# Kernel tuning notes

Hardware: AMD Instinct MI355X
Metric: run time of the kernel (lower is better)

Reference implementation:

```python
import jax, jax.numpy as jnp
import numpy as np

WS = 7
HEADS = 8
DIM = 96
MLP_HIDDEN = 384


def _rel_pos_index(ws):
    coords = np.stack(np.meshgrid(np.arange(ws), np.arange(ws), indexing='ij'))  # (2,ws,ws)
    cf = coords.reshape(2, -1)
    rel = (cf[:, :, None] - cf[:, None, :]).transpose(1, 2, 0).copy()  # (N,N,2)
    rel[..., 0] += ws - 1
    rel[..., 1] += ws - 1
    rel[..., 0] *= 2 * ws - 1
    return rel.sum(-1)  # (N,N)

RPI = jnp.asarray(_rel_pos_index(WS).reshape(-1))


def _window_partition(x, ws):
    B, H, W, C = x.shape
    x = x.reshape(B, H // ws, ws, W // ws, ws, C)
    return x.transpose(0, 1, 3, 2, 4, 5).reshape(-1, ws, ws, C)


def _window_reverse(w, ws, H, W):
    B = w.shape[0] // ((H // ws) * (W // ws))
    x = w.reshape(B, H // ws, W // ws, ws, ws, -1)
    return x.transpose(0, 1, 3, 2, 4, 5).reshape(B, H, W, -1)


def _ln(x, g, b, eps=1e-5):
    m = jnp.mean(x, -1, keepdims=True)
    v = jnp.mean(jnp.square(x - m), -1, keepdims=True)
    return (x - m) * jax.lax.rsqrt(v + eps) * g + b


def _bn(x, g, b, m, v, eps=1e-5):
    # inference-mode BatchNorm2d over NCHW
    s = (g * jax.lax.rsqrt(v + eps))[None, :, None, None]
    return (x - m[None, :, None, None]) * s + b[None, :, None, None]


def _conv(x, w, pad, dil):
    return jax.lax.conv_general_dilated(
        x, w, (1, 1), [(pad, pad), (pad, pad)], rhs_dilation=(dil, dil),
        dimension_numbers=('NCHW', 'OIHW', 'NCHW'))


def forward_impl(x, ndwi_mask, norm1_g, norm1_b, qkv_w, qkv_b, proj_w, proj_b, rpb_table,
                 norm2_g, norm2_b, mlp_w1, mlp_b1, mlp_w2, mlp_b2, norm3_g, norm3_b,
                 conv1_w, conv1_b, bn1_g, bn1_b, bn1_m, bn1_v,
                 conv2_w, conv2_b, bn2_g, bn2_b, bn2_m, bn2_v, H, W):
    B, L, C = x.shape
    ws, heads = WS, HEADS
    shift = ws // 2  # +3 forward shift ('se' direction)
    shortcut = x
    xn = _ln(x, norm1_g, norm1_b).reshape(B, H, W, C)
    sx = jnp.roll(xn, (shift, shift), axis=(1, 2))
    # NDWI-derived additive attention mask (same-region pairs -> 0, else -100)
    nm = jnp.roll(ndwi_mask[:, 0], (shift, shift), axis=(1, 2))  # (B,H,W)
    mw = _window_partition(nm[..., None], ws).reshape(-1, ws * ws)  # (B*nW, N)
    diff = mw[:, None, :] - mw[:, :, None]  # (B*nW, N, N) = mw[:,j]-mw[:,i]
    attn_mask = jnp.where(diff != 0, jnp.float32(-100.0), jnp.float32(0.0)).astype(x.dtype)
    # windowed attention
    xw = _window_partition(sx, ws).reshape(-1, ws * ws, C)
    B_, N, _ = xw.shape
    hd = C // heads
    qkv = (xw @ qkv_w.T + qkv_b).reshape(B_, N, 3, heads, hd).transpose(2, 0, 3, 1, 4)
    q, k, v = qkv[0] * (hd ** -0.5), qkv[1], qkv[2]  # (B_,h,N,hd)
    attn = jnp.einsum('bhnd,bhmd->bhnm', q, k)
    bias = rpb_table[RPI].reshape(N, N, heads).transpose(2, 0, 1)  # (h,N,N)
    attn = attn + bias[None] + attn_mask[:, None]
    attn = jax.nn.softmax(attn, axis=-1)
    out = jnp.einsum('bhnm,bhmd->bhnd', attn, v).transpose(0, 2, 1, 3).reshape(B_, N, C)
    out = out @ proj_w.T + proj_b
    sx = _window_reverse(out.reshape(-1, ws, ws, C), ws, H, W)
    rshift = -ws // 2  # == -4 for ws=7, matches torch's asymmetric reverse shift
    x = jnp.roll(sx, (rshift, rshift), axis=(1, 2)).reshape(B, H * W, C)
    x = shortcut + x
    # MLP
    h = _ln(x, norm2_g, norm2_b)
    h = jax.nn.gelu(h @ mlp_w1.T + mlp_b1, approximate=False) @ mlp_w2.T + mlp_b2
    x = x + h
    # multi-scale CNN branch
    shortcut2 = x
    img = _ln(x, norm3_g, norm3_b).transpose(0, 2, 1).reshape(B, C, H, W)
    h = _conv(img, conv1_w, 1, 1) + conv1_b[None, :, None, None]
    h = jax.nn.gelu(_bn(h, bn1_g, bn1_b, bn1_m, bn1_v), approximate=False)
    h = _conv(h, conv2_w, 2, 2) + conv2_b[None, :, None, None]
    h = jax.nn.gelu(_bn(h, bn2_g, bn2_b, bn2_m, bn2_v), approximate=False)
    h = h.reshape(B, C, H * W).transpose(0, 2, 1)
    return shortcut2 + h


def setup_inputs() -> dict:
    key = jax.random.key(0)
    k = jax.random.split(key, 10)
    B, H, W, C, hid = 4, 224, 224, DIM, MLP_HIDDEN
    std = 0.02
    f32 = jnp.float32
    return {
        'x': jax.random.normal(k[0], (B, H * W, C), f32),
        'ndwi_mask': jax.random.randint(k[1], (B, 1, H, W), 0, 2).astype(f32),
        'norm1_g': jnp.ones((C,), f32), 'norm1_b': jnp.zeros((C,), f32),
        'qkv_w': jax.random.normal(k[2], (3 * C, C), f32) * std, 'qkv_b': jnp.zeros((3 * C,), f32),
        'proj_w': jax.random.normal(k[3], (C, C), f32) * std, 'proj_b': jnp.zeros((C,), f32),
        'rpb_table': jax.random.normal(k[4], ((2 * WS - 1) ** 2, HEADS), f32) * std,
        'norm2_g': jnp.ones((C,), f32), 'norm2_b': jnp.zeros((C,), f32),
        'mlp_w1': jax.random.normal(k[5], (hid, C), f32) * std, 'mlp_b1': jnp.zeros((hid,), f32),
        'mlp_w2': jax.random.normal(k[6], (C, hid), f32) * std, 'mlp_b2': jnp.zeros((C,), f32),
        'norm3_g': jnp.ones((C,), f32), 'norm3_b': jnp.zeros((C,), f32),
        'conv1_w': jax.random.normal(k[7], (C, C, 3, 3), f32) * std, 'conv1_b': jnp.zeros((C,), f32),
        'bn1_g': jnp.ones((C,), f32), 'bn1_b': jnp.zeros((C,), f32),
        'bn1_m': jnp.zeros((C,), f32), 'bn1_v': jnp.ones((C,), f32),
        'conv2_w': jax.random.normal(k[8], (C, C, 3, 3), f32) * std, 'conv2_b': jnp.zeros((C,), f32),
        'bn2_g': jnp.ones((C,), f32), 'bn2_b': jnp.zeros((C,), f32),
        'bn2_m': jnp.zeros((C,), f32), 'bn2_v': jnp.ones((C,), f32),
        'H': H, 'W': W,
    }


def reference(x, ndwi_mask, norm1_g, norm1_b, qkv_w, qkv_b, proj_w, proj_b, rpb_table,
              norm2_g, norm2_b, mlp_w1, mlp_b1, mlp_w2, mlp_b2, norm3_g, norm3_b,
              conv1_w, conv1_b, bn1_g, bn1_b, bn1_m, bn1_v,
              conv2_w, conv2_b, bn2_g, bn2_b, bn2_m, bn2_v, H, W):
    return forward_impl(x, ndwi_mask, norm1_g, norm1_b, qkv_w, qkv_b, proj_w, proj_b, rpb_table,
                        norm2_g, norm2_b, mlp_w1, mlp_b1, mlp_w2, mlp_b2, norm3_g, norm3_b,
                        conv1_w, conv1_b, bn1_g, bn1_b, bn1_m, bn1_v,
                        conv2_w, conv2_b, bn2_g, bn2_b, bn2_m, bn2_v, H, W)
```

## Files before the change

kernel.cpp:

```cpp
#include <hip/hip_runtime.h>
#include <hip/hip_bf16.h>

typedef unsigned int u32;
typedef unsigned short u16;

#define DF __device__ __forceinline__

DF float bf2f(u16 v){ u32 t = ((u32)v)<<16; return __builtin_bit_cast(float, t); }
DF u16 f2bf(float f){
  u32 t = __builtin_bit_cast(u32, f);
  t += 0x7fffu + ((t>>16)&1u);
  return (u16)(t>>16);
}
DF float lo16(u32 p){ return __builtin_bit_cast(float, p<<16); }
DF float hi16(u32 p){ return __builtin_bit_cast(float, p & 0xffff0000u); }
DF u32 pack2(float a, float b){ return (u32)f2bf(a) | (((u32)f2bf(b))<<16); }
DF float gelu(float x){ return 0.5f*x*(1.0f+erff(x*0.70710678118654752f)); }

#if defined(__has_builtin)
#if __has_builtin(__builtin_amdgcn_fdot2_f32_bf16)
#define HAVE_DOT2 1
#endif
#endif
#ifdef HAVE_DOT2
DF float dot2bf(u32 a, u32 b, float c){
  typedef __bf16 b2 __attribute__((ext_vector_type(2)));
  return __builtin_amdgcn_fdot2_f32_bf16(__builtin_bit_cast(b2,a), __builtin_bit_cast(b2,b), c, false);
}
#else
DF float dot2bf(u32 a, u32 b, float c){
  float d;
  asm("v_dot2_f32_bf16 %0, %1, %2, %3" : "=v"(d) : "v"(a), "v"(b), "v"(c));
  return d;
}
#endif

typedef __attribute__((ext_vector_type(8))) __bf16 bf16x8;
typedef __attribute__((ext_vector_type(4))) float f32x4;

__global__ void wprep_k(const float* __restrict__ qkvw, const float* __restrict__ projw,
                        u32* __restrict__ w8q, u32* __restrict__ w8p)
{
  int e = blockIdx.x*256 + threadIdx.x;
  if (e < 13824){
    int jk = e >> 8, lane = (e >> 2) & 63, q = e & 3;
    int jt = jk/3, ks = jk - jt*3;
    int n = jt*16 + (lane & 15);
    int k = ks*32 + (lane >> 4)*8 + 2*q;
    w8q[e] = pack2(qkvw[n*96 + k], qkvw[n*96 + k + 1]);
  } else if (e < 18432){
    int r2 = e - 13824;
    int jk = r2 >> 8, lane = (r2 >> 2) & 63, q = r2 & 3;
    int jt = jk/3, ks = jk - jt*3;
    int n = jt*16 + (lane & 15);
    int k = ks*32 + (lane >> 4)*8 + 2*q;
    w8p[r2] = pack2(projw[n*96 + k], projw[n*96 + k + 1]);
  }
}

__global__ void wprep_cv(const float* __restrict__ c1w, const float* __restrict__ c2w,
                         u32* __restrict__ wcv)
{
  int e = blockIdx.x*256 + threadIdx.x;
  if (e >= 82944) return;
  int conv = e / 41472, r = e - conv*41472;
  int tap = r / 4608, r2 = r - tap*4608;
  int jk = r2 >> 8;
  int lane = (r2 >> 2) & 63;
  int q = r2 & 3;
  int j = jk/3, ks = jk - j*3;
  int n = j*16 + (lane & 15);
  int k = ks*32 + (lane >> 4)*8 + 2*q;
  const float* s = conv ? c2w : c1w;
  wcv[e] = pack2(s[(n*96 + k)*9 + tap], s[(n*96 + k + 1)*9 + tap]);
}

__global__ void wprep_m(const float* __restrict__ w1, const float* __restrict__ w2,
                        u32* __restrict__ wm)
{
  int e = blockIdx.x*256 + threadIdx.x;
  if (e >= 36864) return;
  int which = e / 18432, r = e - which*18432;
  int q = r / 4608, r2 = r - q*4608;
  int jk = r2 >> 8, lane = (r2 >> 2) & 63, qq = r2 & 3;
  int jt = jk/3, ks = jk - jt*3;
  int n = jt*16 + (lane & 15);
  int k = ks*32 + (lane >> 4)*8 + 2*qq;
  if (which == 0){
    const float* s = w1 + (size_t)(q*96 + n)*96 + k;
    wm[e] = pack2(s[0], s[1]);
  } else {
    const float* s = w2 + (size_t)n*384 + q*96 + k;
    wm[e] = pack2(s[0], s[1]);
  }
}

__global__ __launch_bounds__(256,3) void attn_k(
    const float* __restrict__ x, const float* __restrict__ ndwi,
    const float* __restrict__ n1g, const float* __restrict__ n1b,
    const u32* __restrict__ w8q, const float* __restrict__ qb,
    const u32* __restrict__ w8p, const float* __restrict__ pb,
    const float* __restrict__ rpbt, u16* __restrict__ x1o)
{
  __shared__ __align__(16) u16 xA[4*3*64*8];
  __shared__ u32 qp[49*49];
  __shared__ u32 kp[49*49];
  __shared__ u16 vpT[96*50];
  __shared__ float rpb[8*169];
  __shared__ float mw[49];
  const int tid = threadIdx.x;
  const int blk = blockIdx.x;
  const int b = blk >> 10, wy = (blk>>5)&31, wx = blk&31;
  const int wv_ = __builtin_amdgcn_readfirstlane(tid >> 6);
  const int ln  = tid & 63;
  const int colv = ln & 15, rgrp = ln >> 4;

  for (int i = tid; i < 1352; i += 256){
    int h = i/169, idx = i - h*169;
    rpb[i] = rpbt[idx*8 + h];
  }
  for (int i = tid; i < 96; i += 256) vpT[i*50 + 49] = 0;

  if (tid < 196){
    const int t = tid >> 2, p = tid & 3;
    const int ty = t/7, tx = t - (t/7)*7;
    int sy = wy*7 + ty - 3; if (sy < 0) sy += 224;
    int sx = wx*7 + tx - 3; if (sx < 0) sx += 224;
    const size_t rowb = ((size_t)((b*224 + sy)*224 + sx))*96;
    const float* xr = x + rowb + p*24;
    float c[24];
    #pragma unroll
    for (int q = 0; q < 6; q++){
      float4 v = ((const float4*)xr)[q];
      c[q*4+0]=v.x; c[q*4+1]=v.y; c[q*4+2]=v.z; c[q*4+3]=v.w;
    }
    if (p == 0) mw[t] = ndwi[(size_t)b*50176 + sy*224 + sx];
    float s = 0.f, s2 = 0.f;
    #pragma unroll
    for (int j = 0; j < 24; j++){ s += c[j]; s2 += c[j]*c[j]; }
    s  += __shfl_xor(s, 1);  s  += __shfl_xor(s, 2);
    s2 += __shfl_xor(s2, 1); s2 += __shfl_xor(s2, 2);
    float m = s*(1.f/96.f);
    float rs = rsqrtf(s2*(1.f/96.f) - m*m + 1e-5f);
    const int mt = t >> 4, row = t & 15;
    #pragma unroll
    for (int jj = 0; jj < 12; jj++){
      int k = p*24 + 2*jj;
      float a = (c[2*jj]  -m)*rs*n1g[k]   + n1b[k];
      float d = (c[2*jj+1]-m)*rs*n1g[k+1] + n1b[k+1];
      int ks = k >> 5, g = (k & 31) >> 3, i = k & 7;
      *(u32*)&xA[(((mt*3 + ks)*64 + g*16 + row)<<3) + i] = pack2(a, d);
    }
  }
  __syncthreads();

  {
    bf16x8 af[3];
    #pragma unroll
    for (int ks = 0; ks < 3; ks++)
      af[ks] = *(const bf16x8*)&xA[((wv_*3 + ks)*64 + ln)*8];
    u16* qpu = (u16*)qp;
    u16* kpu = (u16*)kp;
    const float S = 0.28867513459481287f;
    for (int jt = 0; jt < 18; jt++){
      f32x4 c = (f32x4){0.f,0.f,0.f,0.f};
      #pragma unroll
      for (int ks = 0; ks < 3; ks++){
        bf16x8 bw = *(const bf16x8*)(w8q + ((jt*3 + ks)*64 + ln)*4);
        c = __builtin_amdgcn_mfma_f32_16x16x32_bf16(af[ks], bw, c, 0, 0, 0);
      }
      const int oc = jt*16 + colv;
      const float bv = qb[oc];
      #pragma unroll
      for (int r = 0; r < 4; r++){
        int tok = wv_*16 + rgrp*4 + r;
        if (tok < 49){
          float v = c[r] + bv;
          if (oc < 96)       qpu[tok*98 + oc]        = f2bf(v*S);
          else if (oc < 192) kpu[tok*98 + (oc-96)]   = f2bf(v);
          else               vpT[(oc-192)*50 + tok]  = f2bf(v);
        }
      }
    }
  }
  __syncthreads();

  for (int task = tid; task < 392; task += 256){
    int h = task/49, i = task - (task/49)*49;
    int iy = i/7, ix = i - (i/7)*7;
    u32 qv[6];
    #pragma unroll
    for (int e = 0; e < 6; e++) qv[e] = qp[i*49 + h*6 + e];
    const float* rb = &rpb[h*169 + (iy+6)*13 + (ix+6)];
    float s[49]; float mx = -1e30f;
    float mi = mw[i];
    int j = 0;
    #pragma unroll
    for (int jy = 0; jy < 7; jy++)
    #pragma unroll
    for (int jx = 0; jx < 7; jx++, j++){
      const u32* kr = &kp[j*49 + h*6];
      float a = rb[-(jy*13+jx)];
      a = dot2bf(qv[0], kr[0], a); a = dot2bf(qv[1], kr[1], a);
      a = dot2bf(qv[2], kr[2], a); a = dot2bf(qv[3], kr[3], a);
      a = dot2bf(qv[4], kr[4], a); a = dot2bf(qv[5], kr[5], a);
      a = (mi != mw[j]) ? a - 100.f : a;
      s[j] = a; mx = fmaxf(mx, a);
    }
    float l = 0.f;
    #pragma unroll
    for (int jj = 0; jj < 49; jj++){ float p = __expf(s[jj]-mx); s[jj] = p; l += p; }
    float rl = 1.f/l;
    u32 pp[25];
    #pragma unroll
    for (int e = 0; e < 24; e++)
      pp[e] = (__builtin_bit_cast(u32, s[2*e]) >> 16)
            | (__builtin_bit_cast(u32, s[2*e+1]) & 0xffff0000u);
    pp[24] = __builtin_bit_cast(u32, s[48]) >> 16;
    float o[12];
    #pragma unroll
    for (int d = 0; d < 12; d++){
      const u32* vr = (const u32*)(vpT + (h*12+d)*50);
      float od = 0.f;
      #pragma unroll
      for (int e = 0; e < 25; e++) od = dot2bf(pp[e], vr[e], od);
      o[d] = od*rl;
    }
    const int mt2 = i >> 4, row2 = i & 15;
    #pragma unroll
    for (int m = 0; m < 6; m++){
      int k = h*12 + 2*m;
      int ks = k >> 5, g = (k & 31) >> 3, ii = k & 7;
      *(u32*)&xA[(((mt2*3 + ks)*64 + g*16 + row2)<<3) + ii] = pack2(o[2*m], o[2*m+1]);
    }
  }
  __syncthreads();

  {
    bf16x8 af[3];
    #pragma unroll
    for (int ks = 0; ks < 3; ks++)
      af[ks] = *(const bf16x8*)&xA[((wv_*3 + ks)*64 + ln)*8];
    u16* qpu = (u16*)qp;
    for (int jt = 0; jt < 6; jt++){
      f32x4 c = (f32x4){0.f,0.f,0.f,0.f};
      #pragma unroll
      for (int ks = 0; ks < 3; ks++){
        bf16x8 bw = *(const bf16x8*)(w8p + ((jt*3 + ks)*64 + ln)*4);
        c = __builtin_amdgcn_mfma_f32_16x16x32_bf16(af[ks], bw, c, 0, 0, 0);
      }
      const int oc = jt*16 + colv;
      const float bv = pb[oc];
      #pragma unroll
      for (int r = 0; r < 4; r++){
        int tok = wv_*16 + rgrp*4 + r;
        if (tok < 49) qpu[tok*98 + oc] = f2bf(c[r] + bv);
      }
    }
  }
  __syncthreads();

  for (int e = tid; e < 588; e += 256){
    int t = e/12, g = e - (e/12)*12;
    int ty = t/7, tx = t - (t/7)*7;
    int dy = wy*7 + ty - 4; if (dy < 0) dy += 224;
    int dx = wx*7 + tx - 4; if (dx < 0) dx += 224;
    size_t base = ((size_t)((b*224+dy)*224+dx))*96 + g*8;
    float4 r0 = *(const float4*)(x + base);
    float4 r1 = *(const float4*)(x + base + 4);
    const u32* pr = &qp[t*49 + g*4];
    uint4 ov;
    ov.x = pack2(lo16(pr[0])+r0.x, hi16(pr[0])+r0.y);
    ov.y = pack2(lo16(pr[1])+r0.z, hi16(pr[1])+r0.w);
    ov.z = pack2(lo16(pr[2])+r1.x, hi16(pr[2])+r1.y);
    ov.w = pack2(lo16(pr[3])+r1.z, hi16(pr[3])+r1.w);
    *(uint4*)(x1o + base) = ov;
  }
}

__global__ __launch_bounds__(256,4) void mlp_direct_k(
    const u16* __restrict__ x1, const u32* __restrict__ wm,
    const float* __restrict__ b1, const float* __restrict__ b2,
    const float* __restrict__ g2, const float* __restrict__ bb2,
    float* __restrict__ x2o)
{
  __shared__ __align__(16) u16 xA[4*3*64*8];
  __shared__ __align__(16) u16 hA[4*3*64*8];
  const int tid = threadIdx.x;
  const size_t t0 = (size_t)blockIdx.x * 64;
  const int wvM = tid >> 6;
  const int ln  = tid & 63;
  const int colv = ln & 15, rgrp = ln >> 4;
  const u32* w1m = wm;
  const u32* w2m = wm + 18432;

  {
    const int t = tid >> 2, p = tid & 3;
    const u16* xr = x1 + (t0 + t)*96 + p*24;
    float c[24];
    #pragma unroll
    for (int q = 0; q < 3; q++){
      uint4 v = ((const uint4*)xr)[q];
      c[q*8+0]=lo16(v.x); c[q*8+1]=hi16(v.x);
      c[q*8+2]=lo16(v.y); c[q*8+3]=hi16(v.y);
      c[q*8+4]=lo16(v.z); c[q*8+5]=hi16(v.z);
      c[q*8+6]=lo16(v.w); c[q*8+7]=hi16(v.w);
    }
    float s = 0.f, s2 = 0.f;
    #pragma unroll
    for (int j = 0; j < 24; j++){ s += c[j]; s2 += c[j]*c[j]; }
    s  += __shfl_xor(s, 1);  s  += __shfl_xor(s, 2);
    s2 += __shfl_xor(s2, 1); s2 += __shfl_xor(s2, 2);
    float m = s*(1.f/96.f);
    float rs = rsqrtf(s2*(1.f/96.f) - m*m + 1e-5f);
    const int mt = t >> 4, row = t & 15;
    #pragma unroll
    for (int jj = 0; jj < 12; jj++){
      int k = p*24 + 2*jj;
      float a = (c[2*jj]  -m)*rs*g2[k]   + bb2[k];
      float d = (c[2*jj+1]-m)*rs*g2[k+1] + bb2[k+1];
      int ks = k >> 5, g = (k & 31) >> 3, i = k & 7;
      *(u32*)&xA[(((mt*3 + ks)*64 + g*16 + row)<<3) + i] = pack2(a, d);
    }
  }
  __syncthreads();

  bf16x8 af[3];
  #pragma unroll
  for (int ks = 0; ks < 3; ks++)
    af[ks] = *(const bf16x8*)&xA[((wvM*3 + ks)*64 + ln)*8];

  f32x4 acc2[6];
  #pragma unroll
  for (int j = 0; j < 6; j++) acc2[j] = (f32x4){0.f,0.f,0.f,0.f};

  for (int q = 0; q < 4; q++){
    __syncthreads();
    #pragma unroll
    for (int j = 0; j < 6; j++){
      f32x4 c = (f32x4){0.f,0.f,0.f,0.f};
      #pragma unroll
      for (int ks = 0; ks < 3; ks++){
        bf16x8 bfv = *(const bf16x8*)(w1m + ((q*18 + j*3 + ks)*64 + ln)*4);
        c = __builtin_amdgcn_mfma_f32_16x16x32_bf16(af[ks], bfv, c, 0, 0, 0);
      }
      const float bv = b1[q*96 + j*16 + colv];
      const int kq = j*16 + colv;
      const int ks2 = kq >> 5, gg = (kq & 31) >> 3, ii = kq & 7;
      u16* hdst = &hA[(((wvM*3 + ks2)*64 + gg*16)<<3) + ii];
      #pragma unroll
      for (int r = 0; r < 4; r++){
        int rowh = rgrp*4 + r;
        hdst[rowh*8] = f2bf(gelu(c[r] + bv));
      }
    }
    __syncthreads();

    bf16x8 hf[3];
    #pragma unroll
    for (int ks = 0; ks < 3; ks++)
      hf[ks] = *(const bf16x8*)&hA[((wvM*3 + ks)*64 + ln)*8];
    #pragma unroll
    for (int j = 0; j < 6; j++){
      #pragma unroll
      for (int ks = 0; ks < 3; ks++){
        bf16x8 bfv = *(const bf16x8*)(w2m + ((q*18 + j*3 + ks)*64 + ln)*4);
        acc2[j] = __builtin_amdgcn_mfma_f32_16x16x32_bf16(hf[ks], bfv, acc2[j], 0, 0, 0);
      }
    }
  }

  #pragma unroll
  for (int j = 0; j < 6; j++){
    const int oc = j*16 + colv;
    const float bv = b2[oc];
    #pragma unroll
    for (int r = 0; r < 4; r++){
      size_t tok = t0 + wvM*16 + rgrp*4 + r;
      x2o[tok*96 + oc] = acc2[j][r] + bv + bf2f(x1[tok*96 + oc]);
    }
  }
}

__global__ __launch_bounds__(256,2) void mlp_stage_k(
    const u16* __restrict__ x1, const float* __restrict__ w1, const float* __restrict__ b1,
    const float* __restrict__ w2, const float* __restrict__ b2,
    const float* __restrict__ g2, const float* __restrict__ bb2,
    float* __restrict__ x2o)
{
  __shared__ __align__(16) u16 xA [4*3*64*8];
  __shared__ __align__(16) u16 hA [4*3*64*8];
  __shared__ __align__(16) u16 w1f[6*3*64*8];
  __shared__ __align__(16) u16 w2f[6*3*64*8];
  const int tid = threadIdx.x;
  const size_t t0 = (size_t)blockIdx.x * 64;
  const int wvM = tid >> 6;
  const int ln  = tid & 63;
  const int colv = ln & 15, rgrp = ln >> 4;

  {
    const int t = tid >> 2, p = tid & 3;
    const u16* xr = x1 + (t0 + t)*96 + p*24;
    float c[24];
    #pragma unroll
    for (int q = 0; q < 3; q++){
      uint4 v = ((const uint4*)xr)[q];
      c[q*8+0]=lo16(v.x); c[q*8+1]=hi16(v.x);
      c[q*8+2]=lo16(v.y); c[q*8+3]=hi16(v.y);
      c[q*8+4]=lo16(v.z); c[q*8+5]=hi16(v.z);
      c[q*8+6]=lo16(v.w); c[q*8+7]=hi16(v.w);
    }
    float s = 0.f, s2 = 0.f;
    #pragma unroll
    for (int j = 0; j < 24; j++){ s += c[j]; s2 += c[j]*c[j]; }
    s  += __shfl_xor(s, 1);  s  += __shfl_xor(s, 2);
    s2 += __shfl_xor(s2, 1); s2 += __shfl_xor(s2, 2);
    float m = s*(1.f/96.f);
    float rs = rsqrtf(s2*(1.f/96.f) - m*m + 1e-5f);
    const int mt = t >> 4, row = t & 15;
    #pragma unroll
    for (int jj = 0; jj < 12; jj++){
      int k = p*24 + 2*jj;
      float a = (c[2*jj]  -m)*rs*g2[k]   + bb2[k];
      float d = (c[2*jj+1]-m)*rs*g2[k+1] + bb2[k+1];
      int ks = k >> 5, g = (k & 31) >> 3, i = k & 7;
      *(u32*)&xA[(((mt*3 + ks)*64 + g*16 + row)<<3) + i] = pack2(a, d);
    }
  }

  f32x4 acc2[6];
  #pragma unroll
  for (int j = 0; j < 6; j++) acc2[j] = (f32x4){0.f,0.f,0.f,0.f};

  for (int q = 0; q < 4; q++){
    __syncthreads();
    for (int e = tid; e < 4608; e += 256){
      int n = e/48, cp = e - (e/48)*48, k = cp*2;
      int ks = k >> 5, g = (k & 31) >> 3, i = k & 7;
      int fidx = ((((n>>4)*3 + ks)*64 + g*16 + (n&15))<<3) + i;
      {
        const float* s = w1 + (size_t)(q*96 + n)*96 + k;
        *(u32*)&w1f[fidx] = pack2(s[0], s[1]);
      }
      {
        const float* s = w2 + (size_t)n*384 + q*96 + k;
        *(u32*)&w2f[fidx] = pack2(s[0], s[1]);
      }
    }
    __syncthreads();

    bf16x8 af[3];
    #pragma unroll
    for (int ks = 0; ks < 3; ks++)
      af[ks] = *(const bf16x8*)&xA[((wvM*3 + ks)*64 + ln)*8];
    #pragma unroll
    for (int j = 0; j < 6; j++){
      f32x4 c = (f32x4){0.f,0.f,0.f,0.f};
      #pragma unroll
      for (int ks = 0; ks < 3; ks++){
        bf16x8 bfv = *(const bf16x8*)&w1f[((j*3 + ks)*64 + ln)*8];
        c = __builtin_amdgcn_mfma_f32_16x16x32_bf16(af[ks], bfv, c, 0, 0, 0);
      }
      const float bv = b1[q*96 + j*16 + colv];
      const int kq = j*16 + colv;
      const int ks2 = kq >> 5, gg = (kq & 31) >> 3, ii = kq & 7;
      u16* hdst = &hA[(((wvM*3 + ks2)*64 + gg*16)<<3) + ii];
      #pragma unroll
      for (int r = 0; r < 4; r++){
        int rowh = rgrp*4 + r;
        hdst[rowh*8] = f2bf(gelu(c[r] + bv));
      }
    }
    __syncthreads();

    bf16x8 hf[3];
    #pragma unroll
    for (int ks = 0; ks < 3; ks++)
      hf[ks] = *(const bf16x8*)&hA[((wvM*3 + ks)*64 + ln)*8];
    #pragma unroll
    for (int j = 0; j < 6; j++){
      #pragma unroll
      for (int ks = 0; ks < 3; ks++){
        bf16x8 bfv = *(const bf16x8*)&w2f[((j*3 + ks)*64 + ln)*8];
        acc2[j] = __builtin_amdgcn_mfma_f32_16x16x32_bf16(hf[ks], bfv, acc2[j], 0, 0, 0);
      }
    }
  }

  #pragma unroll
  for (int j = 0; j < 6; j++){
    const int oc = j*16 + colv;
    const float bv = b2[oc];
    #pragma unroll
    for (int r = 0; r < 4; r++){
      size_t tok = t0 + wvM*16 + rgrp*4 + r;
      x2o[tok*96 + oc] = acc2[j][r] + bv + bf2f(x1[tok*96 + oc]);
    }
  }
}

template<int DIL, bool LN3, bool FINAL, bool WD>
__global__ __launch_bounds__(256,4) void convm_k(
    const void* __restrict__ srcv, const u32* __restrict__ wpk,
    const float* __restrict__ wOIHW,
    const float* __restrict__ cb, const float* __restrict__ bng, const float* __restrict__ bnb,
    const float* __restrict__ bnm, const float* __restrict__ bnv,
    const float* __restrict__ g3, const float* __restrict__ b3,
    const float* resid, void* dstv)
{
  constexpr int SY = 8 + 2*DIL, SX = 8 + 2*DIL, NPIX = SY*SX;
  __shared__ __align__(16) u16 inT[NPIX*104];
  const int tid = threadIdx.x;
  const int bx = blockIdx.x*8, by = blockIdx.y*8, b = blockIdx.z;
  const int gy0 = by - DIL, gx0 = bx - DIL;

  for (int e = tid; e < NPIX*48; e += 256){
    int p = e/48, c2 = e - (e/48)*48;
    int y = p/SX, xx = p - (p/SX)*SX;
    int gy = gy0+y, gx = gx0+xx;
    u32 v = 0;
    if (gy >= 0 && gy < 224 && gx >= 0 && gx < 224){
      size_t idx = ((size_t)((b*224+gy)*224+gx))*96 + c2*2;
      if (LN3){
        float2 rd = *(const float2*)((const float*)srcv + idx);
        v = pack2(rd.x, rd.y);
      } else {
        v = *(const u32*)((const u16*)srcv + idx);
      }
    }
    *(u32*)&inT[p*104 + c2*2] = v;
  }
  __syncthreads();
  if (LN3){
    if (tid < 2*NPIX){
      const int p = tid >> 1, half = tid & 1;
      int y = p/SX, xx = p - (p/SX)*SX;
      int gy = gy0+y, gx = gx0+xx;
      if (gy >= 0 && gy < 224 && gx >= 0 && gx < 224){
        u32* row = (u32*)&inT[p*104] + half*24;
        float c[48];
        #pragma unroll
        for (int i = 0; i < 24; i++){ u32 v = row[i]; c[2*i] = lo16(v); c[2*i+1] = hi16(v); }
        float s = 0.f, s2 = 0.f;
        #pragma unroll
        for (int i = 0; i < 48; i++){ s += c[i]; s2 += c[i]*c[i]; }
        s  += __shfl_xor(s, 1);
        s2 += __shfl_xor(s2, 1);
        float m = s*(1.f/96.f);
        float rs = rsqrtf(s2*(1.f/96.f) - m*m + 1e-5f);
        const int cbase = half*48;
        #pragma unroll
        for (int i = 0; i < 24; i++){
          float a = (c[2*i]  -m)*rs*g3[cbase+2*i]   + b3[cbase+2*i];
          float d = (c[2*i+1]-m)*rs*g3[cbase+2*i+1] + b3[cbase+2*i+1];
          row[i] = pack2(a, d);
        }
      }
    }
    __syncthreads();
  }

  const int wvM = tid >> 6, ln = tid & 63;
  const int colv = ln & 15, rgrp = ln >> 4;
  const int arow = ln & 15;
  const int aoy = wvM*2 + (arow >> 3), aox = arow & 7;

  f32x4 acc[6];
  #pragma unroll
  for (int j = 0; j < 6; j++) acc[j] = (f32x4){0.f,0.f,0.f,0.f};

  if constexpr (WD){
    #pragma unroll 3
    for (int tap = 0; tap < 9; tap++){
      const int ky = tap/3, kx = tap - (tap/3)*3;
      const int p_in = (aoy + ky*DIL)*SX + aox + kx*DIL;
      bf16x8 af[3];
      #pragma unroll
      for (int ks = 0; ks < 3; ks++)
        af[ks] = *(const bf16x8*)&inT[p_in*104 + ks*32 + rgrp*8];
      const u32* wt = wpk + tap*4608;
      #pragma unroll
      for (int j = 0; j < 6; j++){
        #pragma unroll
        for (int ks = 0; ks < 3; ks++){
          bf16x8 bfv = *(const bf16x8*)(wt + ((j*3 + ks)*64 + ln)*4);
          acc[j] = __builtin_amdgcn_mfma_f32_16x16x32_bf16(af[ks], bfv, acc[j], 0, 0, 0);
        }
      }
    }
  } else {
    __shared__ __align__(16) u32 wfr[4608];
    for (int tap = 0; tap < 9; tap++){
      const int ky = tap/3, kx = tap - (tap/3)*3;
      __syncthreads();
      for (int e = tid; e < 4608; e += 256){
        int jk = e >> 8, lane = (e >> 2) & 63, q = e & 3;
        int j = jk/3, ks = jk - j*3;
        int n = j*16 + (lane & 15);
        int k = ks*32 + (lane >> 4)*8 + 2*q;
        wfr[e] = pack2(wOIHW[(n*96 + k)*9 + tap], wOIHW[(n*96 + k + 1)*9 + tap]);
      }
      __syncthreads();
      const int p_in = (aoy + ky*DIL)*SX + aox + kx*DIL;
      bf16x8 af[3];
      #pragma unroll
      for (int ks = 0; ks < 3; ks++)
        af[ks] = *(const bf16x8*)&inT[p_in*104 + ks*32 + rgrp*8];
      #pragma unroll
      for (int j = 0; j < 6; j++){
        #pragma unroll
        for (int ks = 0; ks < 3; ks++){
          bf16x8 bfv = *(const bf16x8*)((const u16*)wfr + ((j*3 + ks)*64 + ln)*8);
          acc[j] = __builtin_amdgcn_mfma_f32_16x16x32_bf16(af[ks], bfv, acc[j], 0, 0, 0);
        }
      }
    }
  }

  #pragma unroll
  for (int j = 0; j < 6; j++){
    const int oc = j*16 + colv;
    const float sc = bng[oc]*rsqrtf(bnv[oc]+1e-5f);
    const float mm = bnm[oc], bb = bnb[oc], cbv = cb[oc];
    #pragma unroll
    for (int r = 0; r < 4; r++){
      const int rowm = rgrp*4 + r;
      const int gy = by + wvM*2 + (rowm >> 3), gx = bx + (rowm & 7);
      size_t idx = ((size_t)((b*224+gy)*224+gx))*96 + oc;
      float t = (acc[j][r] + cbv - mm)*sc + bb;
      float o = gelu(t);
      if (FINAL){
        ((float*)dstv)[idx] = o + resid[idx];
      } else {
        ((u16*)dstv)[idx] = f2bf(o);
      }
    }
  }
}

extern "C" void kernel_launch(void* const* d_in, const int* in_sizes, int n_in,
                              void* d_out, int out_size, void* d_ws, size_t ws_size,
                              hipStream_t stream)
{
  const float* x    = (const float*)d_in[0];
  const float* ndwi = (const float*)d_in[1];
  const float* n1g  = (const float*)d_in[2];
  const float* n1b  = (const float*)d_in[3];
  const float* qkvw = (const float*)d_in[4];
  const float* qkvb = (const float*)d_in[5];
  const float* projw= (const float*)d_in[6];
  const float* projb= (const float*)d_in[7];
  const float* rpbt = (const float*)d_in[8];
  const float* n2g  = (const float*)d_in[9];
  const float* n2b  = (const float*)d_in[10];
  const float* w1   = (const float*)d_in[11];
  const float* b1   = (const float*)d_in[12];
  const float* w2   = (const float*)d_in[13];
  const float* b2   = (const float*)d_in[14];
  const float* n3g  = (const float*)d_in[15];
  const float* n3b  = (const float*)d_in[16];
  const float* c1w  = (const float*)d_in[17];
  const float* c1b  = (const float*)d_in[18];
  const float* bn1g = (const float*)d_in[19];
  const float* bn1b = (const float*)d_in[20];
  const float* bn1m = (const float*)d_in[21];
  const float* bn1v = (const float*)d_in[22];
  const float* c2w  = (const float*)d_in[23];
  const float* c2b  = (const float*)d_in[24];
  const float* bn2g = (const float*)d_in[25];
  const float* bn2b = (const float*)d_in[26];
  const float* bn2m = (const float*)d_in[27];
  const float* bn2v = (const float*)d_in[28];

  int B = out_size / (224*224*96);
  if (B < 1 || B > 64) B = 4;
  const size_t elems = (size_t)B*224*224*96;

  u16*   wsA = (u16*)d_ws;
  u32*   w8q = (u32*)d_out;
  u32*   w8p = w8q + 13824;
  float* xo  = (float*)d_out;
  u32*   wcv = nullptr;
  u32*   wm  = nullptr;
  if (ws_size >= elems*sizeof(u16) + 82944*sizeof(u32))
    wcv = (u32*)(wsA + elems);
  if (ws_size >= elems*sizeof(u16) + (82944 + 36864)*sizeof(u32))
    wm = wcv + 82944;

  wprep_k<<<dim3(72), dim3(256), 0, stream>>>(qkvw, projw, w8q, w8p);
  if (wcv) wprep_cv<<<dim3(324), dim3(256), 0, stream>>>(c1w, c2w, wcv);
  if (wm)  wprep_m<<<dim3(144), dim3(256), 0, stream>>>(w1, w2, wm);
  attn_k<<<dim3(B*1024), dim3(256), 0, stream>>>(x, ndwi, n1g, n1b, w8q, qkvb, w8p, projb, rpbt, wsA);
  if (wm)
    mlp_direct_k<<<dim3(B*784), dim3(256), 0, stream>>>(wsA, wm, b1, b2, n2g, n2b, xo);
  else
    mlp_stage_k<<<dim3(B*784), dim3(256), 0, stream>>>(wsA, w1, b1, w2, b2, n2g, n2b, xo);
  if (wcv){
    convm_k<1,true ,false,true ><<<dim3(28,28,B), dim3(256), 0, stream>>>(
        xo,  wcv,        c1w, c1b, bn1g, bn1b, bn1m, bn1v, n3g, n3b, nullptr, wsA);
    convm_k<2,false,true ,true ><<<dim3(28,28,B), dim3(256), 0, stream>>>(
        wsA, wcv+41472,  c2w, c2b, bn2g, bn2b, bn2m, bn2v, nullptr, nullptr, xo, xo);
  } else {
    convm_k<1,true ,false,false><<<dim3(28,28,B), dim3(256), 0, stream>>>(
        xo,  nullptr,    c1w, c1b, bn1g, bn1b, bn1m, bn1v, n3g, n3b, nullptr, wsA);
    convm_k<2,false,true ,false><<<dim3(28,28,B), dim3(256), 0, stream>>>(
        wsA, nullptr,    c2w, c2b, bn2g, bn2b, bn2m, bn2v, nullptr, nullptr, xo, xo);
  }
}
```

Measured before the change: 555.7 us.

## Compute window attention QK^T and PV with 16x16x16 bf16 MFMA

Replaces the per-thread scalar dot2 attention (one thread per head/query row) with wave-level MFMA tiles for QK^T and PV. K and V are written into MFMA-ready B-operand layouts in shared memory, and the softmax runs on the MFMA accumulators using cross-lane shuffles. Probabilities are staged per wave in LDS. The relative position bias table is stored as bf16 to save LDS. Launch bounds occupancy drops from 3 to 2, and padding of 49 tokens up to 64 wastes some MFMA work and adds bf16 rounding of the probabilities and bias.

```diff
diff --git a/kernel.cpp b/kernel.cpp
--- a/kernel.cpp
+++ b/kernel.cpp
@@ -17,26 +17,32 @@
 DF u32 pack2(float a, float b){ return (u32)f2bf(a) | (((u32)f2bf(b))<<16); }
 DF float gelu(float x){ return 0.5f*x*(1.0f+erff(x*0.70710678118654752f)); }
 
+typedef __attribute__((ext_vector_type(8))) __bf16 bf16x8;
+typedef __attribute__((ext_vector_type(4))) __bf16 bf16x4;
+typedef __attribute__((ext_vector_type(4))) float f32x4;
+
 #if defined(__has_builtin)
-#if __has_builtin(__builtin_amdgcn_fdot2_f32_bf16)
-#define HAVE_DOT2 1
+#if __has_builtin(__builtin_amdgcn_mfma_f32_16x16x16_bf16)
+#define MFMA16_OK 1
+DF f32x4 mfma16(bf16x4 a, bf16x4 b, f32x4 c){
+  return __builtin_amdgcn_mfma_f32_16x16x16_bf16(a, b, c, 0, 0, 0);
+}
+#elif __has_builtin(__builtin_amdgcn_mfma_f32_16x16x16bf16_1k)
+#define MFMA16_OK 1
+typedef __attribute__((ext_vector_type(4))) short s16x4;
+DF f32x4 mfma16(bf16x4 a, bf16x4 b, f32x4 c){
+  return __builtin_amdgcn_mfma_f32_16x16x16bf16_1k(
+      __builtin_bit_cast(s16x4, a), __builtin_bit_cast(s16x4, b), c, 0, 0, 0);
+}
 #endif
 #endif
-#ifdef HAVE_DOT2
-DF float dot2bf(u32 a, u32 b, float c){
-  typedef __bf16 b2 __attribute__((ext_vector_type(2)));
-  return __builtin_amdgcn_fdot2_f32_bf16(__builtin_bit_cast(b2,a), __builtin_bit_cast(b2,b), c, false);
-}
-#else
-DF float dot2bf(u32 a, u32 b, float c){
-  float d;
-  asm("v_dot2_f32_bf16 %0, %1, %2, %3" : "=v"(d) : "v"(a), "v"(b), "v"(c));
+#ifndef MFMA16_OK
+DF f32x4 mfma16(bf16x4 a, bf16x4 b, f32x4 c){
+  f32x4 d;
+  asm("v_mfma_f32_16x16x16_bf16 %0, %1, %2, %3" : "=v"(d) : "v"(a), "v"(b), "v"(c));
   return d;
 }
 #endif
-
-typedef __attribute__((ext_vector_type(8))) __bf16 bf16x8;
-typedef __attribute__((ext_vector_type(4))) float f32x4;
 
 __global__ void wprep_k(const float* __restrict__ qkvw, const float* __restrict__ projw,
                         u32* __restrict__ w8q, u32* __restrict__ w8p)
@@ -95,7 +101,7 @@
   }
 }
 
-__global__ __launch_bounds__(256,3) void attn_k(
+__global__ __launch_bounds__(256,2) void attn_k(
     const float* __restrict__ x, const float* __restrict__ ndwi,
     const float* __restrict__ n1g, const float* __restrict__ n1b,
     const u32* __restrict__ w8q, const float* __restrict__ qb,
@@ -103,10 +109,11 @@
     const float* __restrict__ rpbt, u16* __restrict__ x1o)
 {
   __shared__ __align__(16) u16 xA[4*3*64*8];
-  __shared__ u32 qp[49*49];
-  __shared__ u32 kp[49*49];
-  __shared__ u16 vpT[96*50];
-  __shared__ float rpb[8*169];
+  __shared__ __align__(16) u16 qS[64*100];
+  __shared__ __align__(16) u16 kB[8*4*64*4];
+  __shared__ __align__(16) u16 vB[8*4*64*4];
+  __shared__ __align__(16) u16 pS[4*16*68];
+  __shared__ u16 rpb16[8*169];
   __shared__ float mw[49];
   const int tid = threadIdx.x;
   const int blk = blockIdx.x;
@@ -117,9 +124,10 @@
 
   for (int i = tid; i < 1352; i += 256){
     int h = i/169, idx = i - h*169;
-    rpb[i] = rpbt[idx*8 + h];
-  }
-  for (int i = tid; i < 96; i += 256) vpT[i*50 + 49] = 0;
+    rpb16[i] = f2bf(rpbt[idx*8 + h]);
+  }
+  for (int i = tid; i < 4096; i += 256){ ((u32*)kB)[i] = 0; ((u32*)vB)[i] = 0; }
+  for (int i = tid; i < 3200; i += 256) ((u32*)qS)[i] = 0;
 
   if (tid < 196){
     const int t = tid >> 2, p = tid & 3;
@@ -159,8 +167,6 @@
     #pragma unroll
     for (int ks = 0; ks < 3; ks++)
       af[ks] = *(const bf16x8*)&xA[((wv_*3 + ks)*64 + ln)*8];
-    u16* qpu = (u16*)qp;
-    u16* kpu = (u16*)kp;
     const float S = 0.28867513459481287f;
     for (int jt = 0; jt < 18; jt++){
       f32x4 c = (f32x4){0.f,0.f,0.f,0.f};
@@ -176,62 +182,88 @@
         int tok = wv_*16 + rgrp*4 + r;
         if (tok < 49){
           float v = c[r] + bv;
-          if (oc < 96)       qpu[tok*98 + oc]        = f2bf(v*S);
-          else if (oc < 192) kpu[tok*98 + (oc-96)]   = f2bf(v);
-          else               vpT[(oc-192)*50 + tok]  = f2bf(v);
+          if (oc < 96){
+            qS[tok*100 + oc] = f2bf(v*S);
+          } else if (oc < 192){
+            int ock = oc - 96, h = ock/12, kd = ock - h*12;
+            kB[((h*4 + (tok>>4))*64 + (kd>>2)*16 + (tok&15))*4 + (kd&3)] = f2bf(v);
+          } else {
+            int ocv = oc - 192, h = ocv/12, d = ocv - h*12;
+            vB[((h*4 + (tok>>4))*64 + ((tok&15)>>2)*16 + d)*4 + (tok&3)] = f2bf(v);
+          }
         }
       }
     }
   }
   __syncthreads();
 
-  for (int task = tid; task < 392; task += 256){
-    int h = task/49, i = task - (task/49)*49;
-    int iy = i/7, ix = i - (i/7)*7;
-    u32 qv[6];
-    #pragma unroll
-    for (int e = 0; e < 6; e++) qv[e] = qp[i*49 + h*6 + e];
-    const float* rb = &rpb[h*169 + (iy+6)*13 + (ix+6)];
-    float s[49]; float mx = -1e30f;
-    float mi = mw[i];
-    int j = 0;
-    #pragma unroll
-    for (int jy = 0; jy < 7; jy++)
-    #pragma unroll
-    for (int jx = 0; jx < 7; jx++, j++){
-      const u32* kr = &kp[j*49 + h*6];
-      float a = rb[-(jy*13+jx)];
-      a = dot2bf(qv[0], kr[0], a); a = dot2bf(qv[1], kr[1], a);
-      a = dot2bf(qv[2], kr[2], a); a = dot2bf(qv[3], kr[3], a);
-      a = dot2bf(qv[4], kr[4], a); a = dot2bf(qv[5], kr[5], a);
-      a = (mi != mw[j]) ? a - 100.f : a;
-      s[j] = a; mx = fmaxf(mx, a);
-    }
-    float l = 0.f;
-    #pragma unroll
-    for (int jj = 0; jj < 49; jj++){ float p = __expf(s[jj]-mx); s[jj] = p; l += p; }
-    float rl = 1.f/l;
-    u32 pp[25];
-    #pragma unroll
-    for (int e = 0; e < 24; e++)
-      pp[e] = (__builtin_bit_cast(u32, s[2*e]) >> 16)
-            | (__builtin_bit_cast(u32, s[2*e+1]) & 0xffff0000u);
-    pp[24] = __builtin_bit_cast(u32, s[48]) >> 16;
-    float o[12];
-    #pragma unroll
-    for (int d = 0; d < 12; d++){
-      const u32* vr = (const u32*)(vpT + (h*12+d)*50);
-      float od = 0.f;
-      #pragma unroll
-      for (int e = 0; e < 25; e++) od = dot2bf(pp[e], vr[e], od);
-      o[d] = od*rl;
-    }
-    const int mt2 = i >> 4, row2 = i & 15;
-    #pragma unroll
-    for (int m = 0; m < 6; m++){
-      int k = h*12 + 2*m;
-      int ks = k >> 5, g = (k & 31) >> 3, ii = k & 7;
-      *(u32*)&xA[(((mt2*3 + ks)*64 + g*16 + row2)<<3) + ii] = pack2(o[2*m], o[2*m+1]);
+  {
+    int jyv[4], jxv[4]; float mwj[4]; bool jok[4];
+    #pragma unroll
+    for (int nt = 0; nt < 4; nt++){
+      int j = nt*16 + colv;
+      jok[nt] = (j < 49);
+      int jc = jok[nt] ? j : 48;
+      jyv[nt] = jc/7; jxv[nt] = jc - 7*jyv[nt];
+      mwj[nt] = mw[jc];
+    }
+    u16* pw = pS + wv_*(16*68);
+    for (int hh = 0; hh < 2; hh++){
+      const int h = wv_ + hh*4;
+      for (int mt = 0; mt < 4; mt++){
+        bf16x4 aq = *(const bf16x4*)&qS[(mt*16 + (ln&15))*100 + h*12 + (ln>>4)*4];
+        f32x4 Sm[4];
+        #pragma unroll
+        for (int nt = 0; nt < 4; nt++)
+          Sm[nt] = mfma16(aq, *(const bf16x4*)&kB[((h*4 + nt)*64 + ln)*4],
+                          (f32x4){0.f,0.f,0.f,0.f});
+        #pragma unroll
+        for (int r = 0; r < 4; r++){
+          int i = mt*16 + rgrp*4 + r;
+          int ic = i < 49 ? i : 48;
+          int iy = ic/7, ix = ic - 7*iy;
+          float mi = mw[ic];
+          float val[4]; float mx = -3e38f;
+          #pragma unroll
+          for (int nt = 0; nt < 4; nt++){
+            float a = Sm[nt][r] + bf2f(rpb16[h*169 + (iy - jyv[nt] + 6)*13 + (ix - jxv[nt] + 6)]);
+            a = (mi != mwj[nt]) ? a - 100.f : a;
+            a = jok[nt] ? a : -3e38f;
+            val[nt] = a; mx = fmaxf(mx, a);
+          }
+          mx = fmaxf(mx, __shfl_xor(mx, 1));
+          mx = fmaxf(mx, __shfl_xor(mx, 2));
+          mx = fmaxf(mx, __shfl_xor(mx, 4));
+          mx = fmaxf(mx, __shfl_xor(mx, 8));
+          float p[4]; float l = 0.f;
+          #pragma unroll
+          for (int nt = 0; nt < 4; nt++){ p[nt] = __expf(val[nt]-mx); l += p[nt]; }
+          l += __shfl_xor(l, 1); l += __shfl_xor(l, 2);
+          l += __shfl_xor(l, 4); l += __shfl_xor(l, 8);
+          float rl = 1.f/l;
+          #pragma unroll
+          for (int nt = 0; nt < 4; nt++)
+            pw[(rgrp*4 + r)*68 + nt*16 + colv] = f2bf(p[nt]*rl);
+        }
+        asm volatile("" ::: "memory");
+        f32x4 O = (f32x4){0.f,0.f,0.f,0.f};
+        #pragma unroll
+        for (int ks = 0; ks < 4; ks++){
+          bf16x4 aP = *(const bf16x4*)&pw[(ln&15)*68 + ks*16 + (ln>>4)*4];
+          O = mfma16(aP, *(const bf16x4*)&vB[((h*4 + ks)*64 + ln)*4], O);
+        }
+        asm volatile("" ::: "memory");
+        if (colv < 12){
+          int cch = h*12 + colv;
+          int ks2 = cch >> 5, g2 = (cch & 31) >> 3, ii = cch & 7;
+          #pragma unroll
+          for (int r = 0; r < 4; r++){
+            int tok = mt*16 + rgrp*4 + r;
+            if (tok < 49)
+              xA[(((mt*3 + ks2)*64 + g2*16 + (tok&15))<<3) + ii] = f2bf(O[r]);
+          }
+        }
+      }
     }
   }
   __syncthreads();
@@ -241,7 +273,6 @@
     #pragma unroll
     for (int ks = 0; ks < 3; ks++)
       af[ks] = *(const bf16x8*)&xA[((wv_*3 + ks)*64 + ln)*8];
-    u16* qpu = (u16*)qp;
     for (int jt = 0; jt < 6; jt++){
       f32x4 c = (f32x4){0.f,0.f,0.f,0.f};
       #pragma unroll
@@ -254,12 +285,13 @@
       #pragma unroll
       for (int r = 0; r < 4; r++){
         int tok = wv_*16 + rgrp*4 + r;
-        if (tok < 49) qpu[tok*98 + oc] = f2bf(c[r] + bv);
+        if (tok < 49) qS[tok*100 + oc] = f2bf(c[r] + bv);
       }
     }
   }
   __syncthreads();
 
+  const u32* qS32 = (const u32*)qS;
   for (int e = tid; e < 588; e += 256){
     int t = e/12, g = e - (e/12)*12;
     int ty = t/7, tx = t - (t/7)*7;
@@ -268,7 +300,7 @@
     size_t base = ((size_t)((b*224+dy)*224+dx))*96 + g*8;
     float4 r0 = *(const float4*)(x + base);
     float4 r1 = *(const float4*)(x + base + 4);
-    const u32* pr = &qp[t*49 + g*4];
+    const u32* pr = &qS32[t*50 + g*4];
     uint4 ov;
     ov.x = pack2(lo16(pr[0])+r0.x, hi16(pr[0])+r0.y);
     ov.y = pack2(lo16(pr[1])+r0.z, hi16(pr[1])+r0.w);
```

New measurement: 591.8 us. +6.5%, slower.
